# Optimization experiments

Hardware: AMD Instinct MI355X
Metric: run time of the kernel (lower is better)

## Reference

```python
import jax, jax.numpy as jnp
import numpy as np

H = 1024          # hidden_size
NH = 16           # num_attention_heads
HD = H // NH      # attention_head_size = 64
B, S = 8, 1024
LN_EPS = 1e-12


def setup_inputs() -> dict:
    key = jax.random.key(0)
    ks = jax.random.split(key, 12)
    sc = 0.02
    return {
        "input_tensor": jax.random.normal(ks[0], (B, S, H), dtype=jnp.float32),
        "attention_mask": jnp.zeros((B, S), dtype=jnp.float32),
        # LinearMem params (quantization disabled -> plain Linear, torch layout [out,in])
        "Wq": jax.random.normal(ks[1], (H, H), dtype=jnp.float32) * sc,
        "bq": jnp.zeros((H,), dtype=jnp.float32),
        "Wk": jax.random.normal(ks[2], (H, H), dtype=jnp.float32) * sc,
        "bk": jnp.zeros((H,), dtype=jnp.float32),
        "Wv": jax.random.normal(ks[3], (H, H), dtype=jnp.float32) * sc,
        "bv": jnp.zeros((H,), dtype=jnp.float32),
        "Wo": jax.random.normal(ks[4], (H, H), dtype=jnp.float32) * sc,
        "bo": jnp.zeros((H,), dtype=jnp.float32),
        "ln_gamma": jnp.ones((H,), dtype=jnp.float32),
        "ln_beta": jnp.zeros((H,), dtype=jnp.float32),
    }


def _heads(x):  # [B,S,H] -> [B,NH,S,HD]
    return x.reshape(B, S, NH, HD).transpose(0, 2, 1, 3)


def reference(input_tensor, attention_mask, Wq, bq, Wk, bk, Wv, bv, Wo, bo, ln_gamma, ln_beta):
    # Q/K/V projections (LinearMem with quantization disabled == Linear)
    q = _heads(jnp.einsum('bsh,oh->bso', input_tensor, Wq) + bq)
    k = _heads(jnp.einsum('bsh,oh->bso', input_tensor, Wk) + bk)
    v = _heads(jnp.einsum('bsh,oh->bso', input_tensor, Wv) + bv)
    scores = jnp.einsum('bnqd,bnkd->bnqk', q, k) / np.float32(np.sqrt(HD))
    scores = scores + attention_mask[:, None, None, :]  # additive mask [B,1,1,S]
    probs = jax.nn.softmax(scores, axis=-1)  # dropout = identity in eval
    ctx = jnp.einsum('bnqk,bnkd->bnqd', probs, v)
    ctx = ctx.transpose(0, 2, 1, 3).reshape(B, S, H)
    # output projection + residual LayerNorm (eps=1e-12)
    out = jnp.einsum('bsh,oh->bso', ctx, Wo) + bo
    resid = out + input_tensor
    mu = jnp.mean(resid, axis=-1, keepdims=True)
    var = jnp.mean(jnp.square(resid - mu), axis=-1, keepdims=True)
    return (resid - mu) * jax.lax.rsqrt(var + LN_EPS) * ln_gamma + ln_beta
```

## Files before the change

### kernel.cpp

```cpp
#include <hip/hip_runtime.h>

#define NHh 16

typedef unsigned short ushortT;
typedef __attribute__((ext_vector_type(8))) short short8;
typedef __attribute__((ext_vector_type(4))) float floatx4;

__device__ __forceinline__ ushortT f2bf(float x) {
    union { float f; unsigned int u; } cv; cv.f = x;
    unsigned int u = cv.u;
    unsigned int r = u + 0x7fffu + ((u >> 16) & 1u);
    return (ushortT)(r >> 16);
}

__device__ __forceinline__ unsigned pack2_trunc(float a, float b) {
    union { float f; unsigned u; } ua, ub;
    ua.f = a; ub.f = b;
    return (ub.u & 0xffff0000u) | (ua.u >> 16);
}

__device__ __forceinline__ void gload_lds16(const ushortT* g, ushortT* l) {
    __builtin_amdgcn_global_load_lds(
        (const __attribute__((address_space(1))) void*)g,
        (__attribute__((address_space(3))) void*)l, 16, 0, 0);
}

__global__ __launch_bounds__(256) void cvt_x(const float* __restrict__ in,
                                             ushortT* __restrict__ out, int n4) {
    int i = blockIdx.x * 256 + threadIdx.x;
    if (i >= n4) return;
    float4 f = ((const float4*)in)[i];
    uint2 o;
    o.x = (unsigned)f2bf(f.x) | ((unsigned)f2bf(f.y) << 16);
    o.y = (unsigned)f2bf(f.z) | ((unsigned)f2bf(f.w) << 16);
    ((uint2*)out)[i] = o;
}

__global__ __launch_bounds__(256) void cvt_w(const float* __restrict__ W0, const float* __restrict__ W1,
                                             const float* __restrict__ W2, const float* __restrict__ W3,
                                             ushortT* __restrict__ Wall, ushortT* __restrict__ Wob, int n4) {
    int z = blockIdx.y;
    const float* in = (z == 0) ? W0 : (z == 1) ? W1 : (z == 2) ? W2 : W3;
    ushortT* out = (z < 3) ? (Wall + (size_t)z * 1048576) : Wob;
    int i = blockIdx.x * 256 + threadIdx.x;
    if (i >= n4) return;
    float4 f = ((const float4*)in)[i];
    uint2 o;
    o.x = (unsigned)f2bf(f.x) | ((unsigned)f2bf(f.y) << 16);
    o.y = (unsigned)f2bf(f.z) | ((unsigned)f2bf(f.w) << 16);
    ((uint2*)out)[i] = o;
}

__global__ __launch_bounds__(512, 1) void qkv_st(
        const ushortT* __restrict__ X, const ushortT* __restrict__ Wall,
        const float* __restrict__ b0, const float* __restrict__ b1, const float* __restrict__ b2,
        ushortT* __restrict__ Qo, ushortT* __restrict__ Ko, ushortT* __restrict__ Vo) {
    __shared__ __align__(16) ushortT As[2 * 16384];
    __shared__ __align__(16) ushortT Bs[2 * 12288];

    const int l = blockIdx.x;
    const int xcd = l & 7;
    const int j = l >> 3;
    const int mg = j >> 4;
    const int nt = j & 15;
    const int arow0 = (mg * 8 + xcd) * 256;
    const int brow0 = nt * 192;

    const int tid = threadIdx.x;
    const int lane = tid & 63;
    const int w = tid >> 6;
    const int wr = w >> 2;
    const int wc = w & 3;
    const int qd = lane >> 4, ln = lane & 15;

    const ushortT* srcA[4]; const ushortT* srcB[3];
    int oA[4], oB[3];
#pragma unroll
    for (int k = 0; k < 4; k++) {
        int o = k * 8192 + tid * 16;
        int rowblk = o >> 11, ks = (o >> 10) & 1, r = (o >> 6) & 15;
        int c2 = ((o >> 4) & 3) ^ ((r >> 3) << 1);
        srcA[k] = X + (size_t)(arow0 + rowblk * 16 + r) * 1024 + ks * 32 + c2 * 8;
        oA[k] = o;
    }
#pragma unroll
    for (int k = 0; k < 3; k++) {
        int o = k * 8192 + tid * 16;
        int rowblk = o >> 11, ks = (o >> 10) & 1, r = (o >> 6) & 15;
        int c2 = ((o >> 4) & 3) ^ ((r >> 3) << 1);
        srcB[k] = Wall + (size_t)(brow0 + rowblk * 16 + r) * 1024 + ks * 32 + c2 * 8;
        oB[k] = o;
    }

    floatx4 acc[8][3];
#pragma unroll
    for (int i = 0; i < 8; i++)
#pragma unroll
        for (int jj = 0; jj < 3; jj++) acc[i][jj] = (floatx4){0.f, 0.f, 0.f, 0.f};

#pragma unroll
    for (int k = 0; k < 4; k++) { gload_lds16(srcA[k], As + oA[k] / 2); srcA[k] += 64; }
#pragma unroll
    for (int k = 0; k < 3; k++) { gload_lds16(srcB[k], Bs + oB[k] / 2); srcB[k] += 64; }
    asm volatile("s_waitcnt vmcnt(0)" ::: "memory");
    __builtin_amdgcn_s_barrier();

    const int lnc = ln * 64 + ((qd ^ ((ln >> 3) << 1)) * 16);

    for (int T = 0; T < 16; T++) {
        const char* Ab = (const char*)As + (T & 1) * 32768;
        const char* Bb = (const char*)Bs + (T & 1) * 24576;
        short8 afr[8][2], bfr[3][2];
#pragma unroll
        for (int mi = 0; mi < 8; mi++)
#pragma unroll
            for (int ks = 0; ks < 2; ks++)
                afr[mi][ks] = *(const short8*)(Ab + (wr * 8 + mi) * 2048 + ks * 1024 + lnc);
#pragma unroll
        for (int ni = 0; ni < 3; ni++)
#pragma unroll
            for (int ks = 0; ks < 2; ks++)
                bfr[ni][ks] = *(const short8*)(Bb + (wc * 3 + ni) * 2048 + ks * 1024 + lnc);
        if (T < 15) {
            char* An = (char*)As + ((T + 1) & 1) * 32768;
            char* Bn = (char*)Bs + ((T + 1) & 1) * 24576;
#pragma unroll
            for (int k = 0; k < 4; k++) { gload_lds16(srcA[k], (ushortT*)(An + oA[k])); srcA[k] += 64; }
#pragma unroll
            for (int k = 0; k < 3; k++) { gload_lds16(srcB[k], (ushortT*)(Bn + oB[k])); srcB[k] += 64; }
        }
        __builtin_amdgcn_s_barrier();
        asm volatile("s_waitcnt lgkmcnt(0)" ::: "memory");
        __builtin_amdgcn_sched_barrier(0);
        __builtin_amdgcn_s_setprio(1);
#pragma unroll
        for (int mi = 0; mi < 8; mi++)
#pragma unroll
            for (int ni = 0; ni < 3; ni++)
#pragma unroll
                for (int ks = 0; ks < 2; ks++)
                    acc[mi][ni] = __builtin_amdgcn_mfma_f32_16x16x32_bf16(
                        afr[mi][ks], bfr[ni][ks], acc[mi][ni], 0, 0, 0);
        __builtin_amdgcn_s_setprio(0);
        asm volatile("s_waitcnt vmcnt(0)" ::: "memory");
        __builtin_amdgcn_s_barrier();
    }

#pragma unroll
    for (int ni = 0; ni < 3; ni++) {
        int n = brow0 + wc * 48 + ni * 16 + ln;
        int z = n >> 10;
        int col = n & 1023;
        int h = col >> 6, d = col & 63;
        const float* bias = (z == 0) ? b0 : (z == 1) ? b1 : b2;
        float bb = bias[col];
        if (z == 2) {
#pragma unroll
            for (int mi = 0; mi < 8; mi++) {
                int m = arow0 + wr * 128 + mi * 16 + qd * 4;
                int b = m >> 10, s = m & 1023;
                ushort4 pk;
                pk.x = f2bf(acc[mi][ni][0] + bb);
                pk.y = f2bf(acc[mi][ni][1] + bb);
                pk.z = f2bf(acc[mi][ni][2] + bb);
                pk.w = f2bf(acc[mi][ni][3] + bb);
                *(ushort4*)&Vo[((size_t)(b * NHh + h) * 64 + d) * 1024 + s] = pk;
            }
        } else {
            ushortT* Out = z ? Ko : Qo;
#pragma unroll
            for (int mi = 0; mi < 8; mi++) {
#pragma unroll
                for (int r2 = 0; r2 < 4; r2++) {
                    int m = arow0 + wr * 128 + mi * 16 + qd * 4 + r2;
                    int b = m >> 10, s = m & 1023;
                    Out[(size_t)((b * NHh + h) * 1024 + s) * 64 + d] =
                        f2bf(acc[mi][ni][r2] + bb);
                }
            }
        }
    }
}

__device__ __forceinline__ void gemm_core_256x128(
        const ushortT* __restrict__ Ap, const ushortT* __restrict__ Bp,
        int arow0, int brow0, ushortT* As3, ushortT* Bs3,
        int tid, int wr, int wc, int qd, int ln, floatx4 (&acc)[4][4]) {
    const ushortT* srcA[4]; const ushortT* srcB[2];
    int oA[4], oB[2];
#pragma unroll
    for (int k = 0; k < 4; k++) {
        int o = k * 8192 + tid * 16;
        int rowblk = o >> 11, ks = (o >> 10) & 1, r = (o >> 6) & 15;
        int c2 = ((o >> 4) & 3) ^ ((r >> 3) << 1);
        srcA[k] = Ap + (size_t)(arow0 + rowblk * 16 + r) * 1024 + ks * 32 + c2 * 8;
        oA[k] = o;
    }
#pragma unroll
    for (int k = 0; k < 2; k++) {
        int o = k * 8192 + tid * 16;
        int rowblk = o >> 11, ks = (o >> 10) & 1, r = (o >> 6) & 15;
        int c2 = ((o >> 4) & 3) ^ ((r >> 3) << 1);
        srcB[k] = Bp + (size_t)(brow0 + rowblk * 16 + r) * 1024 + ks * 32 + c2 * 8;
        oB[k] = o;
    }
#pragma unroll
    for (int t = 0; t < 2; t++) {
#pragma unroll
        for (int k = 0; k < 4; k++) {
            gload_lds16(srcA[k], (ushortT*)((char*)As3 + t * 32768 + oA[k]));
            srcA[k] += 64;
        }
#pragma unroll
        for (int k = 0; k < 2; k++) {
            gload_lds16(srcB[k], (ushortT*)((char*)Bs3 + t * 16384 + oB[k]));
            srcB[k] += 64;
        }
    }
    asm volatile("s_waitcnt vmcnt(6)" ::: "memory");
    __builtin_amdgcn_s_barrier();

    const int lnc = ln * 64 + ((qd ^ ((ln >> 3) << 1)) * 16);

    int bi = 0, si = 2;
    for (int T = 0; T < 16; T++) {
        const char* Ab = (const char*)As3 + bi * 32768;
        const char* Bb = (const char*)Bs3 + bi * 16384;
        short8 afr[4][2], bfr[4][2];
#pragma unroll
        for (int mi = 0; mi < 4; mi++)
#pragma unroll
            for (int ks = 0; ks < 2; ks++)
                afr[mi][ks] = *(const short8*)(Ab + (mi * 4 + wr) * 2048 + ks * 1024 + lnc);
#pragma unroll
        for (int ni = 0; ni < 4; ni++)
#pragma unroll
            for (int ks = 0; ks < 2; ks++)
                bfr[ni][ks] = *(const short8*)(Bb + (ni * 2 + wc) * 2048 + ks * 1024 + lnc);
        if (T < 14) {
#pragma unroll
            for (int k = 0; k < 4; k++) {
                gload_lds16(srcA[k], (ushortT*)((char*)As3 + si * 32768 + oA[k]));
                srcA[k] += 64;
            }
#pragma unroll
            for (int k = 0; k < 2; k++) {
                gload_lds16(srcB[k], (ushortT*)((char*)Bs3 + si * 16384 + oB[k]));
                srcB[k] += 64;
            }
        }
        __builtin_amdgcn_s_barrier();
        asm volatile("s_waitcnt lgkmcnt(0)" ::: "memory");
        __builtin_amdgcn_sched_barrier(0);
        __builtin_amdgcn_s_setprio(1);
#pragma unroll
        for (int mi = 0; mi < 4; mi++)
#pragma unroll
            for (int ni = 0; ni < 4; ni++)
#pragma unroll
                for (int ks = 0; ks < 2; ks++)
                    acc[mi][ni] = __builtin_amdgcn_mfma_f32_16x16x32_bf16(
                        afr[mi][ks], bfr[ni][ks], acc[mi][ni], 0, 0, 0);
        __builtin_amdgcn_s_setprio(0);
        if (T < 14) { asm volatile("s_waitcnt vmcnt(6)" ::: "memory"); }
        else        { asm volatile("s_waitcnt vmcnt(0)" ::: "memory"); }
        __builtin_amdgcn_s_barrier();
        bi = (bi == 2) ? 0 : bi + 1;
        si = (si == 2) ? 0 : si + 1;
    }
}

__global__ __launch_bounds__(512, 1) void oproj_gemm3(const ushortT* __restrict__ A,
        const ushortT* __restrict__ Wt, const float* __restrict__ bias, float* __restrict__ Pj) {
    __shared__ __align__(16) ushortT As3[3 * 16384];
    __shared__ __align__(16) ushortT Bs3[3 * 8192];

    const int l = blockIdx.x;
    const int xcd = l & 7;
    const int j = l >> 3;
    const int tid = threadIdx.x;
    const int lane = tid & 63;
    const int w = tid >> 6;
    const int wr = w >> 1, wc = w & 1;
    const int qd = lane >> 4, ln = lane & 15;

    const int arow0 = ((j & 3) * 8 + xcd) * 256;
    const int brow0 = (j >> 2) * 128;

    floatx4 acc[4][4];
#pragma unroll
    for (int i = 0; i < 4; i++)
#pragma unroll
        for (int jj = 0; jj < 4; jj++) acc[i][jj] = (floatx4){0.f, 0.f, 0.f, 0.f};

    gemm_core_256x128(A, Wt, arow0, brow0, As3, Bs3, tid, wr, wc, qd, ln, acc);

#pragma unroll
    for (int ni = 0; ni < 4; ni++) {
        int n = brow0 + ni * 32 + wc * 16 + ln;
        float bb = bias[n];
#pragma unroll
        for (int mi = 0; mi < 4; mi++) {
#pragma unroll
            for (int r2 = 0; r2 < 4; r2++) {
                int m = arow0 + mi * 64 + wr * 16 + qd * 4 + r2;
                Pj[(size_t)m * 1024 + n] = acc[mi][ni][r2] + bb;
            }
        }
    }
}

__global__ __launch_bounds__(512, 4) void attn8(const ushortT* __restrict__ Q,
        const ushortT* __restrict__ K, const ushortT* __restrict__ Vg_t,
        const float* __restrict__ mask, ushortT* __restrict__ ctx) {
    __shared__ __align__(16) ushortT Ks[128 * 64];
    __shared__ __align__(16) ushortT Vt[64 * 128];
    __shared__ __align__(16) ushortT Ps[8][32 * 36];

    const int tid = threadIdx.x;
    const int lane = tid & 63;
    const int w = tid >> 6;
    const int qd = lane >> 4;
    const int ln = lane & 15;
    const int l = blockIdx.x;
    const int bh = l & 127;
    const int b = bh >> 4;
    const int h = bh & 15;
    const int qb = l >> 7;

    const ushortT* Qg = Q + (size_t)bh * 65536;
    const ushortT* Kg = K + (size_t)bh * 65536;
    const ushortT* Vg = Vg_t + (size_t)bh * 65536;
    const float* mrow = mask + b * 1024;
    const float LOG2E = 1.4426950408889634f;
    const float SCL = 0.125f * 1.4426950408889634f;

    short8 qf[2][2];
#pragma unroll
    for (int g = 0; g < 2; g++)
#pragma unroll
        for (int ks = 0; ks < 2; ks++)
            qf[g][ks] = *(const short8*)(Qg + (size_t)(qb * 256 + w * 32 + g * 16 + ln) * 64 + ks * 32 + qd * 8);

    float lst[2] = {0.f, 0.f};
    floatx4 accO[2][4];
#pragma unroll
    for (int g = 0; g < 2; g++)
#pragma unroll
        for (int j = 0; j < 4; j++) accO[g][j] = (floatx4){0.f, 0.f, 0.f, 0.f};

    const int ksr = lane >> 3;
    const int kc  = lane & 7;
    const int vdr = lane >> 4;
    const int vcc = lane & 15;

    for (int kt = 0; kt < 8; ++kt) {
        __syncthreads();

#pragma unroll
        for (int ii = 0; ii < 2; ii++) {
            int i = w * 2 + ii;
            int srow = i * 8 + ksr;
            gload_lds16(Kg + (size_t)(kt * 128 + srow) * 64 + (kc ^ ksr) * 8,
                        Ks + i * 512 + lane * 8);
        }
#pragma unroll
        for (int ii = 0; ii < 2; ii++) {
            int i = w * 2 + ii;
            int d = i * 4 + vdr;
            gload_lds16(Vg + (size_t)d * 1024 + kt * 128 + (vcc ^ (d & 15)) * 8,
                        Vt + i * 512 + lane * 8);
        }

        __syncthreads();

#pragma unroll
        for (int h2 = 0; h2 < 2; ++h2) {
#pragma unroll
            for (int mip = 0; mip < 2; ++mip) {
                floatx4 sv[2][2];
#pragma unroll
                for (int mi2 = 0; mi2 < 2; mi2++)
#pragma unroll
                    for (int g = 0; g < 2; g++) sv[mi2][g] = (floatx4){0.f, 0.f, 0.f, 0.f};
#pragma unroll
                for (int ks = 0; ks < 2; ks++) {
                    short8 af[2];
#pragma unroll
                    for (int mi2 = 0; mi2 < 2; mi2++)
                        af[mi2] = *(const short8*)&Ks[(h2 * 64 + mip * 32 + mi2 * 16 + ln) * 64 +
                                                      (((ks * 4 + qd) ^ (ln & 7)) * 8)];
#pragma unroll
                    for (int mi2 = 0; mi2 < 2; mi2++)
#pragma unroll
                        for (int g = 0; g < 2; g++)
                            sv[mi2][g] = __builtin_amdgcn_mfma_f32_16x16x32_bf16(af[mi2], qf[g][ks], sv[mi2][g], 0, 0, 0);
                }

#pragma unroll
                for (int mi2 = 0; mi2 < 2; mi2++) {
                    floatx4 m4 = *(const floatx4*)(mrow + kt * 128 + h2 * 64 + mip * 32 + mi2 * 16 + qd * 4);
                    floatx4 mm;
                    mm[0] = m4[0] * LOG2E; mm[1] = m4[1] * LOG2E;
                    mm[2] = m4[2] * LOG2E; mm[3] = m4[3] * LOG2E;
#pragma unroll
                    for (int g = 0; g < 2; g++) {
                        float p0 = __builtin_amdgcn_exp2f(sv[mi2][g][0] * SCL + mm[0]);
                        float p1 = __builtin_amdgcn_exp2f(sv[mi2][g][1] * SCL + mm[1]);
                        float p2 = __builtin_amdgcn_exp2f(sv[mi2][g][2] * SCL + mm[2]);
                        float p3 = __builtin_amdgcn_exp2f(sv[mi2][g][3] * SCL + mm[3]);
                        lst[g] += (p0 + p1) + (p2 + p3);
                        uint2 wv;
                        wv.x = pack2_trunc(p0, p1);
                        wv.y = pack2_trunc(p2, p3);
                        *(uint2*)&Ps[w][(g * 16 + ln) * 36 + mi2 * 16 + qd * 4] = wv;
                    }
                }

                short8 ap[2], bv[4];
#pragma unroll
                for (int g = 0; g < 2; g++)
                    ap[g] = *(const short8*)&Ps[w][(g * 16 + ln) * 36 + qd * 8];
#pragma unroll
                for (int j = 0; j < 4; j++)
                    bv[j] = *(const short8*)&Vt[(j * 16 + ln) * 128 +
                                                (((h2 * 8 + mip * 4 + qd) ^ ln) * 8)];
#pragma unroll
                for (int g = 0; g < 2; g++)
#pragma unroll
                    for (int j = 0; j < 4; j++)
                        accO[g][j] = __builtin_amdgcn_mfma_f32_16x16x32_bf16(ap[g], bv[j], accO[g][j], 0, 0, 0);
            }
        }
    }

#pragma unroll
    for (int g = 0; g < 2; g++) {
        lst[g] += __shfl_xor(lst[g], 16, 64);
        lst[g] += __shfl_xor(lst[g], 32, 64);
    }

#pragma unroll
    for (int g = 0; g < 2; g++) {
#pragma unroll
        for (int r = 0; r < 4; r++) {
            float lv = __shfl(lst[g], qd * 4 + r, 64);
            float linv = 1.f / lv;
            int q = qb * 256 + w * 32 + g * 16 + qd * 4 + r;
#pragma unroll
            for (int j = 0; j < 4; j++) {
                int d = j * 16 + ln;
                ctx[((size_t)(b * 1024 + q)) * 1024 + h * 64 + d] = f2bf(accO[g][j][r] * linv);
            }
        }
    }
}

__global__ __launch_bounds__(256) void ln_kernel(const float* __restrict__ Pj, const float* __restrict__ X,
        const float* __restrict__ gamma, const float* __restrict__ beta, float* __restrict__ out) {
    __shared__ float red[8];
    int row = blockIdx.x;
    int t = threadIdx.x;
    const float4 p4 = ((const float4*)(Pj + (size_t)row * 1024))[t];
    const float4 x4 = ((const float4*)(X + (size_t)row * 1024))[t];
    float r0 = p4.x + x4.x, r1 = p4.y + x4.y, r2 = p4.z + x4.z, r3 = p4.w + x4.w;
    float s = r0 + r1 + r2 + r3;
    float ss = r0 * r0 + r1 * r1 + r2 * r2 + r3 * r3;
#pragma unroll
    for (int o = 1; o < 64; o <<= 1) { s += __shfl_xor(s, o, 64); ss += __shfl_xor(ss, o, 64); }
    int w = t >> 6;
    if ((t & 63) == 0) { red[w] = s; red[4 + w] = ss; }
    __syncthreads();
    s = red[0] + red[1] + red[2] + red[3];
    ss = red[4] + red[5] + red[6] + red[7];
    float mu = s * (1.f / 1024.f);
    float var = ss * (1.f / 1024.f) - mu * mu;
    float inv = rsqrtf(var + 1e-12f);
    const float4 g4 = ((const float4*)gamma)[t];
    const float4 b4 = ((const float4*)beta)[t];
    float4 o4;
    o4.x = (r0 - mu) * inv * g4.x + b4.x;
    o4.y = (r1 - mu) * inv * g4.y + b4.y;
    o4.z = (r2 - mu) * inv * g4.z + b4.z;
    o4.w = (r3 - mu) * inv * g4.w + b4.w;
    ((float4*)(out + (size_t)row * 1024))[t] = o4;
}

extern "C" void kernel_launch(void* const* d_in, const int* in_sizes, int n_in,
                              void* d_out, int out_size, void* d_ws, size_t ws_size,
                              hipStream_t stream) {
    const float* x     = (const float*)d_in[0];
    const float* mask  = (const float*)d_in[1];
    const float* Wq    = (const float*)d_in[2];
    const float* bq    = (const float*)d_in[3];
    const float* Wk    = (const float*)d_in[4];
    const float* bk    = (const float*)d_in[5];
    const float* Wv    = (const float*)d_in[6];
    const float* bv    = (const float*)d_in[7];
    const float* Wo    = (const float*)d_in[8];
    const float* bo    = (const float*)d_in[9];
    const float* gamma = (const float*)d_in[10];
    const float* beta  = (const float*)d_in[11];
    float* out = (float*)d_out;

    char* ws = (char*)d_ws;
    ushortT* Xb   = (ushortT*)(ws);
    ushortT* Wall = (ushortT*)(ws + (16u << 20));
    ushortT* Wob  = (ushortT*)(ws + (22u << 20));
    ushortT* Qb   = (ushortT*)(ws + (24u << 20));
    ushortT* Kb   = (ushortT*)(ws + (40u << 20));
    ushortT* Vb   = (ushortT*)(ws + (56u << 20));
    ushortT* Cb   = (ushortT*)(ws);
    float*   Pj   = (float*)(ws + (24u << 20));

    cvt_x<<<8192, 256, 0, stream>>>(x, Xb, 2097152);
    cvt_w<<<dim3(1024, 4), 256, 0, stream>>>(Wq, Wk, Wv, Wo, Wall, Wob, 262144);
    qkv_st<<<512, 512, 0, stream>>>(Xb, Wall, bq, bk, bv, Qb, Kb, Vb);
    attn8<<<512, 512, 0, stream>>>(Qb, Kb, Vb, mask, Cb);
    oproj_gemm3<<<256, 512, 0, stream>>>(Cb, Wob, bo, Pj);
    ln_kernel<<<8192, 256, 0, stream>>>(Pj, x, gamma, beta, out);
}
```

Measured before the change: 262.1 us.

## Software-pipeline LDS fragment reads against MFMA in QKV and O-proj GEMMs

Both GEMM kernels now split each 64-wide K tile into two 32-wide halves held in separate register fragment sets. LDS reads for the next half are issued while MFMAs run on the current half. The o-proj kernel goes from a triple-buffered LDS ring to double buffering with two stages prefetched up front. The aim is to hide LDS read latency behind matrix math rather than stalling on lgkmcnt before each MFMA burst. The cost is an extra full vmcnt(0) wait each iteration and a shallower prefetch depth in o-proj, which may expose global load latency.

```diff
diff --git a/kernel.cpp b/kernel.cpp
--- a/kernel.cpp
+++ b/kernel.cpp
@@ -51,7 +51,7 @@
     ((uint2*)out)[i] = o;
 }
 
-__global__ __launch_bounds__(512, 1) void qkv_st(
+__global__ __launch_bounds__(512, 1) void qkv_pipe(
         const ushortT* __restrict__ X, const ushortT* __restrict__ Wall,
         const float* __restrict__ b0, const float* __restrict__ b1, const float* __restrict__ b2,
         ushortT* __restrict__ Qo, ushortT* __restrict__ Ko, ushortT* __restrict__ Vo) {
@@ -98,52 +98,66 @@
 #pragma unroll
         for (int jj = 0; jj < 3; jj++) acc[i][jj] = (floatx4){0.f, 0.f, 0.f, 0.f};
 
-#pragma unroll
-    for (int k = 0; k < 4; k++) { gload_lds16(srcA[k], As + oA[k] / 2); srcA[k] += 64; }
-#pragma unroll
-    for (int k = 0; k < 3; k++) { gload_lds16(srcB[k], Bs + oB[k] / 2); srcB[k] += 64; }
-    asm volatile("s_waitcnt vmcnt(0)" ::: "memory");
+    auto STAGE = [&](int buf) {
+#pragma unroll
+        for (int k = 0; k < 4; k++) {
+            gload_lds16(srcA[k], (ushortT*)((char*)As + buf * 32768 + oA[k]));
+            srcA[k] += 64;
+        }
+#pragma unroll
+        for (int k = 0; k < 3; k++) {
+            gload_lds16(srcB[k], (ushortT*)((char*)Bs + buf * 24576 + oB[k]));
+            srcB[k] += 64;
+        }
+    };
+
+    const int lnc = ln * 64 + ((qd ^ ((ln >> 3) << 1)) * 16);
+
+    short8 a0[8], bf0[3], a1[8], bf1[3];
+
+    auto RD = [&](short8 (&af)[8], short8 (&bf)[3], const char* Ab, const char* Bb, int ksb) {
+#pragma unroll
+        for (int mi = 0; mi < 8; mi++)
+            af[mi] = *(const short8*)(Ab + (wr * 8 + mi) * 2048 + ksb + lnc);
+#pragma unroll
+        for (int ni = 0; ni < 3; ni++)
+            bf[ni] = *(const short8*)(Bb + (wc * 3 + ni) * 2048 + ksb + lnc);
+    };
+    auto MM = [&](short8 (&af)[8], short8 (&bf)[3]) {
+        __builtin_amdgcn_s_setprio(1);
+#pragma unroll
+        for (int mi = 0; mi < 8; mi++)
+#pragma unroll
+            for (int ni = 0; ni < 3; ni++)
+                acc[mi][ni] = __builtin_amdgcn_mfma_f32_16x16x32_bf16(af[mi], bf[ni], acc[mi][ni], 0, 0, 0);
+        __builtin_amdgcn_s_setprio(0);
+    };
+
+    STAGE(0); STAGE(1);
+    asm volatile("s_waitcnt vmcnt(7)" ::: "memory");
     __builtin_amdgcn_s_barrier();
-
-    const int lnc = ln * 64 + ((qd ^ ((ln >> 3) << 1)) * 16);
+    RD(a0, bf0, (const char*)As, (const char*)Bs, 0);
+    asm volatile("s_waitcnt lgkmcnt(0)" ::: "memory");
+    __builtin_amdgcn_sched_barrier(0);
 
     for (int T = 0; T < 16; T++) {
         const char* Ab = (const char*)As + (T & 1) * 32768;
         const char* Bb = (const char*)Bs + (T & 1) * 24576;
-        short8 afr[8][2], bfr[3][2];
-#pragma unroll
-        for (int mi = 0; mi < 8; mi++)
-#pragma unroll
-            for (int ks = 0; ks < 2; ks++)
-                afr[mi][ks] = *(const short8*)(Ab + (wr * 8 + mi) * 2048 + ks * 1024 + lnc);
-#pragma unroll
-        for (int ni = 0; ni < 3; ni++)
-#pragma unroll
-            for (int ks = 0; ks < 2; ks++)
-                bfr[ni][ks] = *(const short8*)(Bb + (wc * 3 + ni) * 2048 + ks * 1024 + lnc);
-        if (T < 15) {
-            char* An = (char*)As + ((T + 1) & 1) * 32768;
-            char* Bn = (char*)Bs + ((T + 1) & 1) * 24576;
-#pragma unroll
-            for (int k = 0; k < 4; k++) { gload_lds16(srcA[k], (ushortT*)(An + oA[k])); srcA[k] += 64; }
-#pragma unroll
-            for (int k = 0; k < 3; k++) { gload_lds16(srcB[k], (ushortT*)(Bn + oB[k])); srcB[k] += 64; }
-        }
+        const char* An = (const char*)As + ((T + 1) & 1) * 32768;
+        const char* Bn = (const char*)Bs + ((T + 1) & 1) * 24576;
+        RD(a1, bf1, Ab, Bb, 1024);
+        __builtin_amdgcn_sched_barrier(0);
+        MM(a0, bf0);
+        asm volatile("s_waitcnt lgkmcnt(0)" ::: "memory");
+        asm volatile("s_waitcnt vmcnt(0)" ::: "memory");
+        __builtin_amdgcn_sched_barrier(0);
         __builtin_amdgcn_s_barrier();
+        if (T < 14) STAGE(T & 1);
+        if (T < 15) RD(a0, bf0, An, Bn, 0);
+        __builtin_amdgcn_sched_barrier(0);
+        MM(a1, bf1);
         asm volatile("s_waitcnt lgkmcnt(0)" ::: "memory");
         __builtin_amdgcn_sched_barrier(0);
-        __builtin_amdgcn_s_setprio(1);
-#pragma unroll
-        for (int mi = 0; mi < 8; mi++)
-#pragma unroll
-            for (int ni = 0; ni < 3; ni++)
-#pragma unroll
-                for (int ks = 0; ks < 2; ks++)
-                    acc[mi][ni] = __builtin_amdgcn_mfma_f32_16x16x32_bf16(
-                        afr[mi][ks], bfr[ni][ks], acc[mi][ni], 0, 0, 0);
-        __builtin_amdgcn_s_setprio(0);
-        asm volatile("s_waitcnt vmcnt(0)" ::: "memory");
-        __builtin_amdgcn_s_barrier();
     }
 
 #pragma unroll
@@ -182,98 +196,10 @@
     }
 }
 
-__device__ __forceinline__ void gemm_core_256x128(
-        const ushortT* __restrict__ Ap, const ushortT* __restrict__ Bp,
-        int arow0, int brow0, ushortT* As3, ushortT* Bs3,
-        int tid, int wr, int wc, int qd, int ln, floatx4 (&acc)[4][4]) {
-    const ushortT* srcA[4]; const ushortT* srcB[2];
-    int oA[4], oB[2];
-#pragma unroll
-    for (int k = 0; k < 4; k++) {
-        int o = k * 8192 + tid * 16;
-        int rowblk = o >> 11, ks = (o >> 10) & 1, r = (o >> 6) & 15;
-        int c2 = ((o >> 4) & 3) ^ ((r >> 3) << 1);
-        srcA[k] = Ap + (size_t)(arow0 + rowblk * 16 + r) * 1024 + ks * 32 + c2 * 8;
-        oA[k] = o;
-    }
-#pragma unroll
-    for (int k = 0; k < 2; k++) {
-        int o = k * 8192 + tid * 16;
-        int rowblk = o >> 11, ks = (o >> 10) & 1, r = (o >> 6) & 15;
-        int c2 = ((o >> 4) & 3) ^ ((r >> 3) << 1);
-        srcB[k] = Bp + (size_t)(brow0 + rowblk * 16 + r) * 1024 + ks * 32 + c2 * 8;
-        oB[k] = o;
-    }
-#pragma unroll
-    for (int t = 0; t < 2; t++) {
-#pragma unroll
-        for (int k = 0; k < 4; k++) {
-            gload_lds16(srcA[k], (ushortT*)((char*)As3 + t * 32768 + oA[k]));
-            srcA[k] += 64;
-        }
-#pragma unroll
-        for (int k = 0; k < 2; k++) {
-            gload_lds16(srcB[k], (ushortT*)((char*)Bs3 + t * 16384 + oB[k]));
-            srcB[k] += 64;
-        }
-    }
-    asm volatile("s_waitcnt vmcnt(6)" ::: "memory");
-    __builtin_amdgcn_s_barrier();
-
-    const int lnc = ln * 64 + ((qd ^ ((ln >> 3) << 1)) * 16);
-
-    int bi = 0, si = 2;
-    for (int T = 0; T < 16; T++) {
-        const char* Ab = (const char*)As3 + bi * 32768;
-        const char* Bb = (const char*)Bs3 + bi * 16384;
-        short8 afr[4][2], bfr[4][2];
-#pragma unroll
-        for (int mi = 0; mi < 4; mi++)
-#pragma unroll
-            for (int ks = 0; ks < 2; ks++)
-                afr[mi][ks] = *(const short8*)(Ab + (mi * 4 + wr) * 2048 + ks * 1024 + lnc);
-#pragma unroll
-        for (int ni = 0; ni < 4; ni++)
-#pragma unroll
-            for (int ks = 0; ks < 2; ks++)
-                bfr[ni][ks] = *(const short8*)(Bb + (ni * 2 + wc) * 2048 + ks * 1024 + lnc);
-        if (T < 14) {
-#pragma unroll
-            for (int k = 0; k < 4; k++) {
-                gload_lds16(srcA[k], (ushortT*)((char*)As3 + si * 32768 + oA[k]));
-                srcA[k] += 64;
-            }
-#pragma unroll
-            for (int k = 0; k < 2; k++) {
-                gload_lds16(srcB[k], (ushortT*)((char*)Bs3 + si * 16384 + oB[k]));
-                srcB[k] += 64;
-            }
-        }
-        __builtin_amdgcn_s_barrier();
-        asm volatile("s_waitcnt lgkmcnt(0)" ::: "memory");
-        __builtin_amdgcn_sched_barrier(0);
-        __builtin_amdgcn_s_setprio(1);
-#pragma unroll
-        for (int mi = 0; mi < 4; mi++)
-#pragma unroll
-            for (int ni = 0; ni < 4; ni++)
-#pragma unroll
-                for (int ks = 0; ks < 2; ks++)
-                    acc[mi][ni] = __builtin_amdgcn_mfma_f32_16x16x32_bf16(
-                        afr[mi][ks], bfr[ni][ks], acc[mi][ni], 0, 0, 0);
-        __builtin_amdgcn_s_setprio(0);
-        if (T < 14) { asm volatile("s_waitcnt vmcnt(6)" ::: "memory"); }
-        else        { asm volatile("s_waitcnt vmcnt(0)" ::: "memory"); }
-        __builtin_amdgcn_s_barrier();
-        bi = (bi == 2) ? 0 : bi + 1;
-        si = (si == 2) ? 0 : si + 1;
-    }
-}
-
-__global__ __launch_bounds__(512, 1) void oproj_gemm3(const ushortT* __restrict__ A,
+__global__ __launch_bounds__(512, 1) void oproj_pipe(const ushortT* __restrict__ A,
         const ushortT* __restrict__ Wt, const float* __restrict__ bias, float* __restrict__ Pj) {
-    __shared__ __align__(16) ushortT As3[3 * 16384];
-    __shared__ __align__(16) ushortT Bs3[3 * 8192];
+    __shared__ __align__(16) ushortT As[2 * 16384];
+    __shared__ __align__(16) ushortT Bs[2 * 8192];
 
     const int l = blockIdx.x;
     const int xcd = l & 7;
@@ -287,13 +213,92 @@
     const int arow0 = ((j & 3) * 8 + xcd) * 256;
     const int brow0 = (j >> 2) * 128;
 
+    const ushortT* srcA[4]; const ushortT* srcB[2];
+    int oA[4], oB[2];
+#pragma unroll
+    for (int k = 0; k < 4; k++) {
+        int o = k * 8192 + tid * 16;
+        int rowblk = o >> 11, ks = (o >> 10) & 1, r = (o >> 6) & 15;
+        int c2 = ((o >> 4) & 3) ^ ((r >> 3) << 1);
+        srcA[k] = A + (size_t)(arow0 + rowblk * 16 + r) * 1024 + ks * 32 + c2 * 8;
+        oA[k] = o;
+    }
+#pragma unroll
+    for (int k = 0; k < 2; k++) {
+        int o = k * 8192 + tid * 16;
+        int rowblk = o >> 11, ks = (o >> 10) & 1, r = (o >> 6) & 15;
+        int c2 = ((o >> 4) & 3) ^ ((r >> 3) << 1);
+        srcB[k] = Wt + (size_t)(brow0 + rowblk * 16 + r) * 1024 + ks * 32 + c2 * 8;
+        oB[k] = o;
+    }
+
     floatx4 acc[4][4];
 #pragma unroll
     for (int i = 0; i < 4; i++)
 #pragma unroll
         for (int jj = 0; jj < 4; jj++) acc[i][jj] = (floatx4){0.f, 0.f, 0.f, 0.f};
 
-    gemm_core_256x128(A, Wt, arow0, brow0, As3, Bs3, tid, wr, wc, qd, ln, acc);
+    auto STAGE = [&](int buf) {
+#pragma unroll
+        for (int k = 0; k < 4; k++) {
+            gload_lds16(srcA[k], (ushortT*)((char*)As + buf * 32768 + oA[k]));
+            srcA[k] += 64;
+        }
+#pragma unroll
+        for (int k = 0; k < 2; k++) {
+            gload_lds16(srcB[k], (ushortT*)((char*)Bs + buf * 16384 + oB[k]));
+            srcB[k] += 64;
+        }
+    };
+
+    const int lnc = ln * 64 + ((qd ^ ((ln >> 3) << 1)) * 16);
+
+    short8 a0[4], bf0[4], a1[4], bf1[4];
+
+    auto RD = [&](short8 (&af)[4], short8 (&bf)[4], const char* Ab, const char* Bb, int ksb) {
+#pragma unroll
+        for (int mi = 0; mi < 4; mi++)
+            af[mi] = *(const short8*)(Ab + (mi * 4 + wr) * 2048 + ksb + lnc);
+#pragma unroll
+        for (int ni = 0; ni < 4; ni++)
+            bf[ni] = *(const short8*)(Bb + (ni * 2 + wc) * 2048 + ksb + lnc);
+    };
+    auto MM = [&](short8 (&af)[4], short8 (&bf)[4]) {
+        __builtin_amdgcn_s_setprio(1);
+#pragma unroll
+        for (int mi = 0; mi < 4; mi++)
+#pragma unroll
+            for (int ni = 0; ni < 4; ni++)
+                acc[mi][ni] = __builtin_amdgcn_mfma_f32_16x16x32_bf16(af[mi], bf[ni], acc[mi][ni], 0, 0, 0);
+        __builtin_amdgcn_s_setprio(0);
+    };
+
+    STAGE(0); STAGE(1);
+    asm volatile("s_waitcnt vmcnt(6)" ::: "memory");
+    __builtin_amdgcn_s_barrier();
+    RD(a0, bf0, (const char*)As, (const char*)Bs, 0);
+    asm volatile("s_waitcnt lgkmcnt(0)" ::: "memory");
+    __builtin_amdgcn_sched_barrier(0);
+
+    for (int T = 0; T < 16; T++) {
+        const char* Ab = (const char*)As + (T & 1) * 32768;
+        const char* Bb = (const char*)Bs + (T & 1) * 16384;
+        const char* An = (const char*)As + ((T + 1) & 1) * 32768;
+        const char* Bn = (const char*)Bs + ((T + 1) & 1) * 16384;
+        RD(a1, bf1, Ab, Bb, 1024);
+        __builtin_amdgcn_sched_barrier(0);
+        MM(a0, bf0);
+        asm volatile("s_waitcnt lgkmcnt(0)" ::: "memory");
+        asm volatile("s_waitcnt vmcnt(0)" ::: "memory");
+        __builtin_amdgcn_sched_barrier(0);
+        __builtin_amdgcn_s_barrier();
+        if (T < 14) STAGE(T & 1);
+        if (T < 15) RD(a0, bf0, An, Bn, 0);
+        __builtin_amdgcn_sched_barrier(0);
+        MM(a1, bf1);
+        asm volatile("s_waitcnt lgkmcnt(0)" ::: "memory");
+        __builtin_amdgcn_sched_barrier(0);
+    }
 
 #pragma unroll
     for (int ni = 0; ni < 4; ni++) {
@@ -515,8 +520,8 @@
 
     cvt_x<<<8192, 256, 0, stream>>>(x, Xb, 2097152);
     cvt_w<<<dim3(1024, 4), 256, 0, stream>>>(Wq, Wk, Wv, Wo, Wall, Wob, 262144);
-    qkv_st<<<512, 512, 0, stream>>>(Xb, Wall, bq, bk, bv, Qb, Kb, Vb);
+    qkv_pipe<<<512, 512, 0, stream>>>(Xb, Wall, bq, bk, bv, Qb, Kb, Vb);
     attn8<<<512, 512, 0, stream>>>(Qb, Kb, Vb, mask, Cb);
-    oproj_gemm3<<<256, 512, 0, stream>>>(Cb, Wob, bo, Pj);
+    oproj_pipe<<<256, 512, 0, stream>>>(Cb, Wob, bo, Pj);
     ln_kernel<<<8192, 256, 0, stream>>>(Pj, x, gamma, beta, out);
 }
```

New measurement: 272.2 us. 1.04x slower.

## Double-buffer QKV fragments across k-halves, fuse conversions, move residual into oproj

Applied to the files above, without the earlier changes.

The QKV GEMM main loop is restructured to preload two LDS stages and split each K tile into two halves with register double-buffering, so LDS fragment reads overlap with MFMA issue. The separate input and weight bf16 conversion kernels are merged into a single launch. The residual add moves from the layernorm kernel into the output projection epilogue, so layernorm reads one tensor instead of two. The epilogue now performs strided fp32 reads of x, which may cost some bandwidth.

```diff
diff --git a/kernel.cpp b/kernel.cpp
--- a/kernel.cpp
+++ b/kernel.cpp
@@ -25,10 +25,20 @@
         (__attribute__((address_space(3))) void*)l, 16, 0, 0);
 }
 
-__global__ __launch_bounds__(256) void cvt_x(const float* __restrict__ in,
-                                             ushortT* __restrict__ out, int n4) {
-    int i = blockIdx.x * 256 + threadIdx.x;
-    if (i >= n4) return;
+__global__ __launch_bounds__(256) void cvt_all(const float* __restrict__ x,
+        const float* __restrict__ W0, const float* __restrict__ W1,
+        const float* __restrict__ W2, const float* __restrict__ W3,
+        ushortT* __restrict__ Xb, ushortT* __restrict__ Wall, ushortT* __restrict__ Wob) {
+    int bid = blockIdx.x;
+    const float* in; ushortT* out; int i;
+    if (bid < 8192) {
+        in = x; out = Xb; i = bid * 256 + threadIdx.x;
+    } else {
+        int z = (bid - 8192) >> 10;
+        in = (z == 0) ? W0 : (z == 1) ? W1 : (z == 2) ? W2 : W3;
+        out = (z < 3) ? (Wall + (size_t)z * 1048576) : Wob;
+        i = ((bid - 8192) & 1023) * 256 + threadIdx.x;
+    }
     float4 f = ((const float4*)in)[i];
     uint2 o;
     o.x = (unsigned)f2bf(f.x) | ((unsigned)f2bf(f.y) << 16);
@@ -36,22 +46,7 @@
     ((uint2*)out)[i] = o;
 }
 
-__global__ __launch_bounds__(256) void cvt_w(const float* __restrict__ W0, const float* __restrict__ W1,
-                                             const float* __restrict__ W2, const float* __restrict__ W3,
-                                             ushortT* __restrict__ Wall, ushortT* __restrict__ Wob, int n4) {
-    int z = blockIdx.y;
-    const float* in = (z == 0) ? W0 : (z == 1) ? W1 : (z == 2) ? W2 : W3;
-    ushortT* out = (z < 3) ? (Wall + (size_t)z * 1048576) : Wob;
-    int i = blockIdx.x * 256 + threadIdx.x;
-    if (i >= n4) return;
-    float4 f = ((const float4*)in)[i];
-    uint2 o;
-    o.x = (unsigned)f2bf(f.x) | ((unsigned)f2bf(f.y) << 16);
-    o.y = (unsigned)f2bf(f.z) | ((unsigned)f2bf(f.w) << 16);
-    ((uint2*)out)[i] = o;
-}
-
-__global__ __launch_bounds__(512, 1) void qkv_st(
+__global__ __launch_bounds__(512, 1) void qkv_pipe(
         const ushortT* __restrict__ X, const ushortT* __restrict__ Wall,
         const float* __restrict__ b0, const float* __restrict__ b1, const float* __restrict__ b2,
         ushortT* __restrict__ Qo, ushortT* __restrict__ Ko, ushortT* __restrict__ Vo) {
@@ -98,52 +93,66 @@
 #pragma unroll
         for (int jj = 0; jj < 3; jj++) acc[i][jj] = (floatx4){0.f, 0.f, 0.f, 0.f};
 
-#pragma unroll
-    for (int k = 0; k < 4; k++) { gload_lds16(srcA[k], As + oA[k] / 2); srcA[k] += 64; }
-#pragma unroll
-    for (int k = 0; k < 3; k++) { gload_lds16(srcB[k], Bs + oB[k] / 2); srcB[k] += 64; }
-    asm volatile("s_waitcnt vmcnt(0)" ::: "memory");
+    auto STAGE = [&](int buf) {
+#pragma unroll
+        for (int k = 0; k < 4; k++) {
+            gload_lds16(srcA[k], (ushortT*)((char*)As + buf * 32768 + oA[k]));
+            srcA[k] += 64;
+        }
+#pragma unroll
+        for (int k = 0; k < 3; k++) {
+            gload_lds16(srcB[k], (ushortT*)((char*)Bs + buf * 24576 + oB[k]));
+            srcB[k] += 64;
+        }
+    };
+
+    const int lnc = ln * 64 + ((qd ^ ((ln >> 3) << 1)) * 16);
+
+    short8 a0[8], bf0[3], a1[8], bf1[3];
+
+    auto RD = [&](short8 (&af)[8], short8 (&bf)[3], const char* Ab, const char* Bb, int ksb) {
+#pragma unroll
+        for (int mi = 0; mi < 8; mi++)
+            af[mi] = *(const short8*)(Ab + (wr * 8 + mi) * 2048 + ksb + lnc);
+#pragma unroll
+        for (int ni = 0; ni < 3; ni++)
+            bf[ni] = *(const short8*)(Bb + (wc * 3 + ni) * 2048 + ksb + lnc);
+    };
+    auto MM = [&](short8 (&af)[8], short8 (&bf)[3]) {
+        __builtin_amdgcn_s_setprio(1);
+#pragma unroll
+        for (int mi = 0; mi < 8; mi++)
+#pragma unroll
+            for (int ni = 0; ni < 3; ni++)
+                acc[mi][ni] = __builtin_amdgcn_mfma_f32_16x16x32_bf16(af[mi], bf[ni], acc[mi][ni], 0, 0, 0);
+        __builtin_amdgcn_s_setprio(0);
+    };
+
+    STAGE(0); STAGE(1);
+    asm volatile("s_waitcnt vmcnt(7)" ::: "memory");
     __builtin_amdgcn_s_barrier();
-
-    const int lnc = ln * 64 + ((qd ^ ((ln >> 3) << 1)) * 16);
+    RD(a0, bf0, (const char*)As, (const char*)Bs, 0);
+    asm volatile("s_waitcnt lgkmcnt(0)" ::: "memory");
+    __builtin_amdgcn_sched_barrier(0);
 
     for (int T = 0; T < 16; T++) {
         const char* Ab = (const char*)As + (T & 1) * 32768;
         const char* Bb = (const char*)Bs + (T & 1) * 24576;
-        short8 afr[8][2], bfr[3][2];
-#pragma unroll
-        for (int mi = 0; mi < 8; mi++)
-#pragma unroll
-            for (int ks = 0; ks < 2; ks++)
-                afr[mi][ks] = *(const short8*)(Ab + (wr * 8 + mi) * 2048 + ks * 1024 + lnc);
-#pragma unroll
-        for (int ni = 0; ni < 3; ni++)
-#pragma unroll
-            for (int ks = 0; ks < 2; ks++)
-                bfr[ni][ks] = *(const short8*)(Bb + (wc * 3 + ni) * 2048 + ks * 1024 + lnc);
-        if (T < 15) {
-            char* An = (char*)As + ((T + 1) & 1) * 32768;
-            char* Bn = (char*)Bs + ((T + 1) & 1) * 24576;
-#pragma unroll
-            for (int k = 0; k < 4; k++) { gload_lds16(srcA[k], (ushortT*)(An + oA[k])); srcA[k] += 64; }
-#pragma unroll
-            for (int k = 0; k < 3; k++) { gload_lds16(srcB[k], (ushortT*)(Bn + oB[k])); srcB[k] += 64; }
-        }
+        const char* An = (const char*)As + ((T + 1) & 1) * 32768;
+        const char* Bn = (const char*)Bs + ((T + 1) & 1) * 24576;
+        RD(a1, bf1, Ab, Bb, 1024);
+        __builtin_amdgcn_sched_barrier(0);
+        MM(a0, bf0);
+        asm volatile("s_waitcnt lgkmcnt(0)" ::: "memory");
+        asm volatile("s_waitcnt vmcnt(0)" ::: "memory");
+        __builtin_amdgcn_sched_barrier(0);
         __builtin_amdgcn_s_barrier();
+        if (T < 14) STAGE(T & 1);
+        if (T < 15) RD(a0, bf0, An, Bn, 0);
+        __builtin_amdgcn_sched_barrier(0);
+        MM(a1, bf1);
         asm volatile("s_waitcnt lgkmcnt(0)" ::: "memory");
         __builtin_amdgcn_sched_barrier(0);
-        __builtin_amdgcn_s_setprio(1);
-#pragma unroll
-        for (int mi = 0; mi < 8; mi++)
-#pragma unroll
-            for (int ni = 0; ni < 3; ni++)
-#pragma unroll
-                for (int ks = 0; ks < 2; ks++)
-                    acc[mi][ni] = __builtin_amdgcn_mfma_f32_16x16x32_bf16(
-                        afr[mi][ks], bfr[ni][ks], acc[mi][ni], 0, 0, 0);
-        __builtin_amdgcn_s_setprio(0);
-        asm volatile("s_waitcnt vmcnt(0)" ::: "memory");
-        __builtin_amdgcn_s_barrier();
     }
 
 #pragma unroll
@@ -271,7 +280,8 @@
 }
 
 __global__ __launch_bounds__(512, 1) void oproj_gemm3(const ushortT* __restrict__ A,
-        const ushortT* __restrict__ Wt, const float* __restrict__ bias, float* __restrict__ Pj) {
+        const ushortT* __restrict__ Wt, const float* __restrict__ bias,
+        const float* __restrict__ Xf, float* __restrict__ Pj) {
     __shared__ __align__(16) ushortT As3[3 * 16384];
     __shared__ __align__(16) ushortT Bs3[3 * 8192];
 
@@ -304,7 +314,7 @@
 #pragma unroll
             for (int r2 = 0; r2 < 4; r2++) {
                 int m = arow0 + mi * 64 + wr * 16 + qd * 4 + r2;
-                Pj[(size_t)m * 1024 + n] = acc[mi][ni][r2] + bb;
+                Pj[(size_t)m * 1024 + n] = acc[mi][ni][r2] + bb + Xf[(size_t)m * 1024 + n];
             }
         }
     }
@@ -456,14 +466,13 @@
     }
 }
 
-__global__ __launch_bounds__(256) void ln_kernel(const float* __restrict__ Pj, const float* __restrict__ X,
+__global__ __launch_bounds__(256) void ln_res(const float* __restrict__ Pj,
         const float* __restrict__ gamma, const float* __restrict__ beta, float* __restrict__ out) {
     __shared__ float red[8];
     int row = blockIdx.x;
     int t = threadIdx.x;
     const float4 p4 = ((const float4*)(Pj + (size_t)row * 1024))[t];
-    const float4 x4 = ((const float4*)(X + (size_t)row * 1024))[t];
-    float r0 = p4.x + x4.x, r1 = p4.y + x4.y, r2 = p4.z + x4.z, r3 = p4.w + x4.w;
+    float r0 = p4.x, r1 = p4.y, r2 = p4.z, r3 = p4.w;
     float s = r0 + r1 + r2 + r3;
     float ss = r0 * r0 + r1 * r1 + r2 * r2 + r3 * r3;
 #pragma unroll
@@ -513,10 +522,9 @@
     ushortT* Cb   = (ushortT*)(ws);
     float*   Pj   = (float*)(ws + (24u << 20));
 
-    cvt_x<<<8192, 256, 0, stream>>>(x, Xb, 2097152);
-    cvt_w<<<dim3(1024, 4), 256, 0, stream>>>(Wq, Wk, Wv, Wo, Wall, Wob, 262144);
-    qkv_st<<<512, 512, 0, stream>>>(Xb, Wall, bq, bk, bv, Qb, Kb, Vb);
+    cvt_all<<<12288, 256, 0, stream>>>(x, Wq, Wk, Wv, Wo, Xb, Wall, Wob);
+    qkv_pipe<<<512, 512, 0, stream>>>(Xb, Wall, bq, bk, bv, Qb, Kb, Vb);
     attn8<<<512, 512, 0, stream>>>(Qb, Kb, Vb, mask, Cb);
-    oproj_gemm3<<<256, 512, 0, stream>>>(Cb, Wob, bo, Pj);
-    ln_kernel<<<8192, 256, 0, stream>>>(Pj, x, gamma, beta, out);
-}
+    oproj_gemm3<<<256, 512, 0, stream>>>(Cb, Wob, bo, x, Pj);
+    ln_res<<<8192, 256, 0, stream>>>(Pj, gamma, beta, out);
+}
```

Measured after the change: 267.9 us. 1.02x slower.
